# Performance work log

Hardware: AMD Instinct MI355X
Metric: run time of the kernel (lower is better)

## Reference

```python
import jax, jax.numpy as jnp
import numpy as np

L, B, D = 8192, 4096, 1024


def setup_inputs() -> dict:
    key = jax.random.key(0)
    k1, k2, k3, k4 = jax.random.split(key, 4)
    return {
        "q_hat": jax.random.normal(k1, (L, D), dtype=jnp.float32),
        "q_real": jax.random.normal(k2, (L, D), dtype=jnp.float32),
        "encoded_gt": jax.random.normal(k3, (B, D), dtype=jnp.float32),
        "encoded_pred": jax.random.normal(k4, (B, D), dtype=jnp.float32),
    }


def reference(q_hat, q_real, encoded_gt, encoded_pred):
    # local_loss: -(1/L) * sum_i dot(q_hat[i], q_real[i])
    # (replaces the Python loop of L tiny torch.dot launches with one fused reduce)
    local = -jnp.mean(jnp.sum(q_hat * q_real, axis=-1))

    # global_loss: sum_{i,j} max(0, <pred_i, gt_j> - <pred_i, gt_i> + 1)
    # (replaces the O(B^2) double loop of torch.dot calls with one GEMM)
    scores = jnp.einsum("id,jd->ij", encoded_pred, encoded_gt)  # [B, B]
    pos = jnp.diagonal(scores)                                   # [B]
    margin = jnp.float32(1.0)
    glob = jnp.sum(jnp.maximum(0.0, scores - pos[:, None] + margin))

    return local + glob
```

## Files before the change

kernel.cpp:

```cpp
#include <hip/hip_runtime.h>
#include <hip/hip_bf16.h>

#define LROWS 8192
#define BROWS 4096
#define DDIM  1024

typedef __attribute__((ext_vector_type(4))) float f32x4;

typedef const unsigned int __attribute__((address_space(1))) gu32;
typedef unsigned int       __attribute__((address_space(3))) su32;

__device__ inline unsigned int pack_fp8x4(float4 v) {
    unsigned int w = 0;
    w = __builtin_amdgcn_cvt_pk_fp8_f32(v.x, v.y, w, false);
    w = __builtin_amdgcn_cvt_pk_fp8_f32(v.z, v.w, w, true);
    return w;
}

__global__ __launch_bounds__(256) void prep_kernel(
    const float4* __restrict__ pred,
    const float4* __restrict__ gt,
    unsigned int* __restrict__ opred,
    unsigned int* __restrict__ ogt,
    const float4* __restrict__ qh,
    const float4* __restrict__ qr,
    float* __restrict__ pos,
    float* __restrict__ lpart,
    float* __restrict__ out) {
    __shared__ float sred[4], sred2[4];
    const int row = blockIdx.x;
    const int t = threadIdx.x;
    if (row == 0 && t == 0) out[0] = 0.0f;

    const int idx = row * 256 + t;
    float4 p = pred[idx];
    float4 g = gt[idx];
    opred[idx] = pack_fp8x4(p);
    ogt[idx]   = pack_fp8x4(g);
    float s = p.x * g.x + p.y * g.y + p.z * g.z + p.w * g.w;

    const int qi = row * 512 + t;
    float4 a0 = qh[qi], b0 = qr[qi];
    float4 a1 = qh[qi + 256], b1 = qr[qi + 256];
    float ls = a0.x * b0.x + a0.y * b0.y + a0.z * b0.z + a0.w * b0.w
             + a1.x * b1.x + a1.y * b1.y + a1.z * b1.z + a1.w * b1.w;

    #pragma unroll
    for (int o = 32; o > 0; o >>= 1) {
        s  += __shfl_down(s, o, 64);
        ls += __shfl_down(ls, o, 64);
    }
    if ((t & 63) == 0) { sred[t >> 6] = s; sred2[t >> 6] = ls; }
    __syncthreads();
    if (t == 0) {
        pos[row]   = sred[0] + sred[1] + sred[2] + sred[3];
        lpart[row] = sred2[0] + sred2[1] + sred2[2] + sred2[3];
    }
}

__global__ __launch_bounds__(256) void hinge_gemm(
    const unsigned char* __restrict__ A,
    const unsigned char* __restrict__ Bm,
    const float* __restrict__ pos,
    const float* __restrict__ lpart,
    float* __restrict__ out) {
    __shared__ unsigned char As[128 * 32];
    __shared__ unsigned char Bs[128 * 32];
    __shared__ float pos_s[128];
    __shared__ float sred[4];

    const int bm = blockIdx.y;
    const int bn = blockIdx.x;
    const int tid = threadIdx.x;
    const int lane = tid & 63;
    const int wave = tid >> 6;
    const int wm = wave >> 1;
    const int wn = wave & 1;

    if (tid < 128) pos_s[tid] = pos[bm * 128 + tid];

    const int srow = wave * 32 + (lane >> 1);
    const int scol = (lane & 1) * 16;

    const unsigned char* Abase = A + (size_t)(bm * 128) * DDIM;
    const unsigned char* Bbase = Bm + (size_t)(bn * 128) * DDIM;

    f32x4 zero = {0.0f, 0.0f, 0.0f, 0.0f};
    f32x4 acc[4][4];
    #pragma unroll
    for (int i = 0; i < 4; i++)
        #pragma unroll
        for (int j = 0; j < 4; j++) acc[i][j] = zero;

    const int rsel = lane & 15;
    const int koff = (lane >> 4) * 8;

    for (int k0 = 0; k0 < DDIM; k0 += 32) {
        __builtin_amdgcn_global_load_lds(
            (gu32*)(Abase + (size_t)srow * DDIM + k0 + scol),
            (su32*)(As + wave * 1024), 16, 0, 0);
        __builtin_amdgcn_global_load_lds(
            (gu32*)(Bbase + (size_t)srow * DDIM + k0 + scol),
            (su32*)(Bs + wave * 1024), 16, 0, 0);
        __syncthreads();

        long af[4], bg[4];
        #pragma unroll
        for (int mt = 0; mt < 4; mt++)
            af[mt] = *(const long*)&As[(wm * 64 + mt * 16 + rsel) * 32 + koff];
        #pragma unroll
        for (int nt = 0; nt < 4; nt++)
            bg[nt] = *(const long*)&Bs[(wn * 64 + nt * 16 + rsel) * 32 + koff];
        #pragma unroll
        for (int mt = 0; mt < 4; mt++)
            #pragma unroll
            for (int nt = 0; nt < 4; nt++)
                acc[mt][nt] = __builtin_amdgcn_mfma_f32_16x16x32_fp8_fp8(
                    af[mt], bg[nt], acc[mt][nt], 0, 0, 0);
        __syncthreads();
    }

    float s = 0.0f;
    const int rowq = (lane >> 4) * 4;
    #pragma unroll
    for (int mt = 0; mt < 4; mt++) {
        #pragma unroll
        for (int nt = 0; nt < 4; nt++) {
            #pragma unroll
            for (int r = 0; r < 4; r++) {
                int lr = wm * 64 + mt * 16 + rowq + r;
                float v = acc[mt][nt][r] - pos_s[lr] + 1.0f;
                s += fmaxf(v, 0.0f);
            }
        }
    }
    #pragma unroll
    for (int o = 32; o > 0; o >>= 1) s += __shfl_down(s, o, 64);
    if (lane == 0) sred[wave] = s;
    __syncthreads();
    if (tid == 0) {
        const int bid = (bm * 32 + bn) * 4;
        float lp = lpart[bid] + lpart[bid + 1] + lpart[bid + 2] + lpart[bid + 3];
        atomicAdd(out, sred[0] + sred[1] + sred[2] + sred[3]
                       - lp * (1.0f / (float)LROWS));
    }
}

extern "C" void kernel_launch(void* const* d_in, const int* in_sizes, int n_in,
                              void* d_out, int out_size, void* d_ws, size_t ws_size,
                              hipStream_t stream) {
    const float* q_hat  = (const float*)d_in[0];
    const float* q_real = (const float*)d_in[1];
    const float* gt     = (const float*)d_in[2];
    const float* pred   = (const float*)d_in[3];
    float* out = (float*)d_out;

    char* ws = (char*)d_ws;
    unsigned char* pred_8 = (unsigned char*)ws;
    unsigned char* gt_8   = (unsigned char*)(ws + (size_t)BROWS * DDIM);
    float* pos   = (float*)(ws + (size_t)2 * BROWS * DDIM);
    float* lpart = (float*)(ws + (size_t)2 * BROWS * DDIM + BROWS * 4);

    hipLaunchKernelGGL(prep_kernel, dim3(BROWS), dim3(256), 0, stream,
                       (const float4*)pred, (const float4*)gt,
                       (unsigned int*)pred_8, (unsigned int*)gt_8,
                       (const float4*)q_hat, (const float4*)q_real,
                       pos, lpart, out);

    hipLaunchKernelGGL(hinge_gemm, dim3(32, 32), dim3(256), 0, stream,
                       pred_8, gt_8, pos, lpart, out);
}
```

Baseline: 163.2 us.

## Use scaled 32x32x64 FP8 MFMA with 128-wide K tiles and XOR-swizzled LDS

Swaps the 16x16x32 fp8 MFMA for the gfx950 scaled 32x32x64 f8f6f4 MFMA with unit scales. The K-step per LDS stage grows from 32 to 128 bytes, so there are fewer barriers and loads per tile. The LDS layout uses an XOR swizzle on 16-byte chunks to avoid bank conflicts on the 16-byte fragment reads. The larger LDS tiles and 16-wide accumulators raise register and LDS use, and the epilogue row mapping has to match the 32x32 output layout.

```diff
diff --git a/kernel.cpp b/kernel.cpp
--- a/kernel.cpp
+++ b/kernel.cpp
@@ -5,7 +5,9 @@
 #define BROWS 4096
 #define DDIM  1024
 
-typedef __attribute__((ext_vector_type(4))) float f32x4;
+typedef __attribute__((ext_vector_type(4)))  int   i32x4;
+typedef __attribute__((ext_vector_type(8)))  int   i32x8;
+typedef __attribute__((ext_vector_type(16))) float f32x16;
 
 typedef const unsigned int __attribute__((address_space(1))) gu32;
 typedef unsigned int       __attribute__((address_space(3))) su32;
@@ -64,8 +66,8 @@
     const float* __restrict__ pos,
     const float* __restrict__ lpart,
     float* __restrict__ out) {
-    __shared__ unsigned char As[128 * 32];
-    __shared__ unsigned char Bs[128 * 32];
+    __shared__ unsigned char As[128 * 128];
+    __shared__ unsigned char Bs[128 * 128];
     __shared__ float pos_s[128];
     __shared__ float sred[4];
 
@@ -79,57 +81,79 @@
 
     if (tid < 128) pos_s[tid] = pos[bm * 128 + tid];
 
-    const int srow = wave * 32 + (lane >> 1);
-    const int scol = (lane & 1) * 16;
+    const int grow = lane >> 3;
+    const int usw  = (lane & 7) ^ grow;
 
     const unsigned char* Abase = A + (size_t)(bm * 128) * DDIM;
     const unsigned char* Bbase = Bm + (size_t)(bn * 128) * DDIM;
 
-    f32x4 zero = {0.0f, 0.0f, 0.0f, 0.0f};
-    f32x4 acc[4][4];
+    f32x16 acc[2][2];
     #pragma unroll
-    for (int i = 0; i < 4; i++)
+    for (int i = 0; i < 2; i++)
         #pragma unroll
-        for (int j = 0; j < 4; j++) acc[i][j] = zero;
+        for (int j = 0; j < 2; j++)
+            #pragma unroll
+            for (int r = 0; r < 16; r++) acc[i][j][r] = 0.0f;
 
-    const int rsel = lane & 15;
-    const int koff = (lane >> 4) * 8;
+    const int sc1 = 0x7f7f7f7f;
+    const int mrow = lane & 31;
+    const int kh = lane >> 5;
 
-    for (int k0 = 0; k0 < DDIM; k0 += 32) {
-        __builtin_amdgcn_global_load_lds(
-            (gu32*)(Abase + (size_t)srow * DDIM + k0 + scol),
-            (su32*)(As + wave * 1024), 16, 0, 0);
-        __builtin_amdgcn_global_load_lds(
-            (gu32*)(Bbase + (size_t)srow * DDIM + k0 + scol),
-            (su32*)(Bs + wave * 1024), 16, 0, 0);
+    for (int k0 = 0; k0 < DDIM; k0 += 128) {
+        #pragma unroll
+        for (int i = 0; i < 4; i++) {
+            int c = wave * 4 + i;
+            int row = c * 8 + grow;
+            __builtin_amdgcn_global_load_lds(
+                (gu32*)(Abase + (size_t)row * DDIM + k0 + usw * 16),
+                (su32*)(As + c * 1024), 16, 0, 0);
+            __builtin_amdgcn_global_load_lds(
+                (gu32*)(Bbase + (size_t)row * DDIM + k0 + usw * 16),
+                (su32*)(Bs + c * 1024), 16, 0, 0);
+        }
         __syncthreads();
 
-        long af[4], bg[4];
         #pragma unroll
-        for (int mt = 0; mt < 4; mt++)
-            af[mt] = *(const long*)&As[(wm * 64 + mt * 16 + rsel) * 32 + koff];
-        #pragma unroll
-        for (int nt = 0; nt < 4; nt++)
-            bg[nt] = *(const long*)&Bs[(wn * 64 + nt * 16 + rsel) * 32 + koff];
-        #pragma unroll
-        for (int mt = 0; mt < 4; mt++)
+        for (int h = 0; h < 2; h++) {
+            const int u0 = h * 4 + kh * 2;
+            i32x8 af[2], bg[2];
             #pragma unroll
-            for (int nt = 0; nt < 4; nt++)
-                acc[mt][nt] = __builtin_amdgcn_mfma_f32_16x16x32_fp8_fp8(
-                    af[mt], bg[nt], acc[mt][nt], 0, 0, 0);
+            for (int mt = 0; mt < 2; mt++) {
+                int r = wm * 64 + mt * 32 + mrow;
+                i32x4 x0 = *(const i32x4*)&As[r * 128 + ((u0    ) ^ (r & 7)) * 16];
+                i32x4 x1 = *(const i32x4*)&As[r * 128 + ((u0 + 1) ^ (r & 7)) * 16];
+                af[mt] = __builtin_shufflevector(x0, x1, 0, 1, 2, 3, 4, 5, 6, 7);
+            }
+            #pragma unroll
+            for (int nt = 0; nt < 2; nt++) {
+                int r = wn * 64 + nt * 32 + mrow;
+                i32x4 x0 = *(const i32x4*)&Bs[r * 128 + ((u0    ) ^ (r & 7)) * 16];
+                i32x4 x1 = *(const i32x4*)&Bs[r * 128 + ((u0 + 1) ^ (r & 7)) * 16];
+                bg[nt] = __builtin_shufflevector(x0, x1, 0, 1, 2, 3, 4, 5, 6, 7);
+            }
+            #pragma unroll
+            for (int mt = 0; mt < 2; mt++)
+                #pragma unroll
+                for (int nt = 0; nt < 2; nt++)
+                    acc[mt][nt] = __builtin_amdgcn_mfma_scale_f32_32x32x64_f8f6f4(
+                        af[mt], bg[nt], acc[mt][nt],
+                        0, 0,
+                        0, sc1,
+                        0, sc1);
+        }
         __syncthreads();
     }
 
     float s = 0.0f;
-    const int rowq = (lane >> 4) * 4;
+    const int rq = 4 * (lane >> 5);
     #pragma unroll
-    for (int mt = 0; mt < 4; mt++) {
+    for (int mt = 0; mt < 2; mt++) {
         #pragma unroll
-        for (int nt = 0; nt < 4; nt++) {
+        for (int nt = 0; nt < 2; nt++) {
             #pragma unroll
-            for (int r = 0; r < 4; r++) {
-                int lr = wm * 64 + mt * 16 + rowq + r;
-                float v = acc[mt][nt][r] - pos_s[lr] + 1.0f;
+            for (int i = 0; i < 16; i++) {
+                int lr = wm * 64 + mt * 32 + (i & 3) + 8 * (i >> 2) + rq;
+                float v = acc[mt][nt][i] - pos_s[lr] + 1.0f;
                 s += fmaxf(v, 0.0f);
             }
         }
```

New measurement: 146.6 us (median of 2 runs). 10.1% less time.
